# Kernel tuning notes

Hardware: AMD Instinct MI355X
Metric: run time of the kernel (lower is better)

Reference implementation:

```python
import jax, jax.numpy as jnp
import numpy as np

N_NODES = 50000
N_EDGES = 400000
N_GRAPHS = 1024
HEADS = 2
HID = 312


def gat_conv(x, src, dst, W, a_src, a_dst, bias, n):
    # PyG GATConv, concat=False (mean over heads), negative_slope=0.2,
    # self-loops already included in (src, dst). Eval mode (no dropout).
    h = (x @ W).reshape(n, HEADS, -1)                      # [N,H,C]
    s_src = (h * a_src[None]).sum(-1)                      # [N,H]
    s_dst = (h * a_dst[None]).sum(-1)                      # [N,H]
    alpha = jax.nn.leaky_relu(s_src[src] + s_dst[dst], 0.2)  # [E,H]
    m = jax.ops.segment_max(alpha, dst, num_segments=n)
    e = jnp.exp(alpha - m[dst])
    z = jax.ops.segment_sum(e, dst, num_segments=n)
    coef = e / (z[dst] + 1e-16)                            # edge softmax over dst
    msg = h[src] * coef[:, :, None]                        # [E,H,C]
    out = jax.ops.segment_sum(msg, dst, num_segments=n)    # [N,H,C]
    return out.mean(axis=1) + bias


def setup_inputs() -> dict:
    key = jax.random.key(0)
    ks = jax.random.split(key, 32)
    d = {}
    d['mol_x'] = jax.random.normal(ks[0], (N_NODES, 78), jnp.float32)
    d['mol_edge_index'] = jax.random.randint(ks[1], (2, N_EDGES), 0, N_NODES, jnp.int32)
    d['mol_batch'] = jnp.sort(jax.random.randint(ks[2], (N_NODES,), 0, N_GRAPHS, jnp.int32))
    sc = 0.05
    d['W0'] = jax.random.normal(ks[3], (78, HEADS * HID)) * sc
    d['as0'] = jax.random.normal(ks[4], (HEADS, HID)) * sc
    d['ad0'] = jax.random.normal(ks[5], (HEADS, HID)) * sc
    d['b0'] = jax.random.normal(ks[6], (HID,)) * sc
    d['W1'] = jax.random.normal(ks[7], (HID, HEADS * HID)) * sc
    d['as1'] = jax.random.normal(ks[8], (HEADS, HID)) * sc
    d['ad1'] = jax.random.normal(ks[9], (HEADS, HID)) * sc
    d['b1'] = jax.random.normal(ks[10], (HID,)) * sc
    d['W2'] = jax.random.normal(ks[11], (HID, HEADS * HID)) * sc
    d['as2'] = jax.random.normal(ks[12], (HEADS, HID)) * sc
    d['ad2'] = jax.random.normal(ks[13], (HEADS, HID)) * sc
    d['b2'] = jax.random.normal(ks[14], (HID,)) * sc
    d['fc1_w'] = jax.random.normal(ks[15], (HID, HID)) * sc
    d['fc1_b'] = jax.random.normal(ks[16], (HID,)) * sc
    d['fc2_w'] = jax.random.normal(ks[17], (HID, HID)) * sc
    d['fc2_b'] = jax.random.normal(ks[18], (HID,)) * sc
    d['mol_bias'] = jax.random.uniform(ks[19], (1, HID), minval=-0.2, maxval=0.2)
    d['g1_w'] = jax.random.normal(ks[20], (HID, 1024)) * sc
    d['g1_b'] = jax.random.normal(ks[21], (1024,)) * sc
    d['g2_w'] = jax.random.normal(ks[22], (1024, 128)) * sc
    d['g2_b'] = jax.random.normal(ks[23], (128,)) * sc
    return d


def reference(mol_x, mol_edge_index, mol_batch,
              W0, as0, ad0, b0, W1, as1, ad1, b1, W2, as2, ad2, b2,
              fc1_w, fc1_b, fc2_w, fc2_b, mol_bias,
              g1_w, g1_b, g2_w, g2_b):
    n = mol_x.shape[0]
    loops = jnp.arange(n, dtype=mol_edge_index.dtype)
    src = jnp.concatenate([mol_edge_index[0], loops])
    dst = jnp.concatenate([mol_edge_index[1], loops])

    x1 = jax.nn.relu(gat_conv(mol_x, src, dst, W0, as0, ad0, b0, n))
    h = x1
    for (W, a_s, a_d, b, act) in [(W1, as1, ad1, b1, True), (W2, as2, ad2, b2, False)]:
        x = gat_conv(h, src, dst, W, a_s, a_d, b, n)
        if act:
            x = jax.nn.relu(x)
        z = jax.nn.sigmoid(x @ fc1_w + fc1_b + h @ fc2_w + fc2_b + mol_bias)
        h = z * x + (1 - z) * h

    # global mean pool over graphs
    sums = jax.ops.segment_sum(h, mol_batch, num_segments=N_GRAPHS)
    cnt = jax.ops.segment_sum(jnp.ones((n,), h.dtype), mol_batch, num_segments=N_GRAPHS)
    pooled = sums / jnp.maximum(cnt, 1.0)[:, None]

    out = jax.nn.relu(pooled @ g1_w + g1_b)
    out = out @ g2_w + g2_b  # dropout = identity (eval)
    return out
```

## Files before the change

kernel.cpp:

```cpp
#include <hip/hip_runtime.h>
#include <cstdint>
#include <cstddef>

#define NNODES 50000
#define NEDGE0 400000
#define NETOT  450000
#define NGRAPH 1024
#define CH     312
#define HC     624
#define MP     50048
#define KPA    320
#define AST    640
#define KP0    128
#define GW1    1024

typedef __attribute__((ext_vector_type(4))) float f32x4;
typedef __attribute__((ext_vector_type(8))) short s16x8;

__device__ __forceinline__ unsigned short f2bf(float x) {
  union { float f; unsigned u; } v; v.f = x;
  unsigned r = v.u + 0x7fffu + ((v.u >> 16) & 1u);
  return (unsigned short)(r >> 16);
}
__device__ __forceinline__ float bf2f(unsigned short u) {
  union { unsigned u; float f; } v; v.u = ((unsigned)u) << 16;
  return v.f;
}
__device__ __forceinline__ void gl_lds16(const unsigned short* g, unsigned short* l) {
  __builtin_amdgcn_global_load_lds(
      (const __attribute__((address_space(1))) unsigned int*)g,
      (__attribute__((address_space(3))) unsigned int*)l, 16, 0, 0);
}

__global__ void cvt0_k(const float* __restrict__ in, unsigned short* __restrict__ out) {
  int i = blockIdx.x * blockDim.x + threadIdx.x;
  if (i >= MP * KP0) return;
  int n = i >> 7, c = i & 127;
  out[i] = (n < NNODES && c < 78) ? f2bf(in[(size_t)n * 78 + c]) : (unsigned short)0;
}

__global__ void tcast_k(const float* __restrict__ in, unsigned short* __restrict__ out,
                        int K, int N, int KP_, int NP_) {
  int i = blockIdx.x * blockDim.x + threadIdx.x;
  if (i >= NP_ * KP_) return;
  int n = i / KP_, k = i - n * KP_;
  out[i] = (n < N && k < K) ? f2bf(in[(size_t)k * N + n]) : (unsigned short)0;
}

__global__ void combcast_k(const float* __restrict__ W, unsigned short* __restrict__ out,
                           int K, int KX) {
  int i = blockIdx.x * blockDim.x + threadIdx.x;
  int W2 = 2 * KX;
  if (i >= 384 * W2) return;
  int n = i / W2, k = i - n * W2;
  float v = 0.f;
  if (n < CH) {
    int hd = (k >= KX) ? 1 : 0;
    int kk = hd ? k - KX : k;
    if (kk < K) v = 0.5f * W[(size_t)kk * HC + hd * CH + n];
  }
  out[i] = f2bf(v);
}

__global__ void wafill_k(const float* __restrict__ W, const float* __restrict__ a_s,
                         const float* __restrict__ a_d, float* __restrict__ wa,
                         int K, int KX) {
  int tid = blockIdx.x * blockDim.x + threadIdx.x;
  if (tid >= 4 * KX) return;
  int j = tid / KX, k = tid - j * KX;
  int hd = j & 1;
  const float* a = (j < 2) ? a_s : a_d;
  float s = 0.f;
  if (k < K)
    for (int c = 0; c < CH; ++c)
      s += W[(size_t)k * HC + hd * CH + c] * a[hd * CH + c];
  wa[j * KX + k] = s;
}

__global__ void tcast2_k(const float* __restrict__ fc1, const float* __restrict__ fc2,
                         unsigned short* __restrict__ out) {
  int i = blockIdx.x * blockDim.x + threadIdx.x;
  if (i >= 384 * AST) return;
  int n = i / AST, k = i - n * AST;
  float v = 0.f;
  if (n < CH) {
    if (k < CH) v = fc1[(size_t)k * CH + n];
    else if (k >= KPA && k - KPA < CH) v = fc2[(size_t)(k - KPA) * CH + n];
  }
  out[i] = f2bf(v);
}

__global__ void biasprep_k(const float* __restrict__ b0_, const float* __restrict__ b1_,
                           const float* __restrict__ b2_, const float* __restrict__ fc1b,
                           const float* __restrict__ fc2b, const float* __restrict__ mb,
                           float* __restrict__ bp0, float* __restrict__ bp1,
                           float* __restrict__ bp2, float* __restrict__ gb) {
  int i = blockIdx.x * blockDim.x + threadIdx.x;
  if (i >= 4 * KPA) return;
  int seg = i / KPA, c = i - seg * KPA;
  bool in = c < CH;
  if (seg == 0)      bp0[c] = in ? b0_[c] : 0.f;
  else if (seg == 1) bp1[c] = in ? b1_[c] : 0.f;
  else if (seg == 2) bp2[c] = in ? b2_[c] : 0.f;
  else               gb[c]  = in ? (fc1b[c] + fc2b[c] + mb[c]) : 0.f;
}

__global__ __launch_bounds__(256) void gemm_bb(
    const unsigned short* __restrict__ A, int lda,
    const unsigned short* __restrict__ Bt,
    unsigned short* __restrict__ Cb, float* __restrict__ Cf,
    const float* __restrict__ bias,
    const unsigned short* __restrict__ Xg, const unsigned short* __restrict__ Hg,
    int M, int N, int KP_, int ldc, int act, int gx)
{
  const int nwg = gridDim.x, orig = blockIdx.x;
  const int q = nwg >> 3, r = nwg & 7;
  const int xcd = orig & 7, loc = orig >> 3;
  const int swz = (xcd < r ? xcd * (q + 1) : r * (q + 1) + (xcd - r) * q) + loc;
  const int bn = (swz % gx) * 64, bm = (swz / gx) * 128;

  __shared__ __align__(16) char smem[49152];
  unsigned short* As = (unsigned short*)smem;
  unsigned short* Bs = (unsigned short*)(smem + 32768);
  const int tid = threadIdx.x, lane = tid & 63, w = tid >> 6;
  const int rr = lane >> 3;
  const int cc8 = (lane & 7) ^ rr;

  const int nkt = KP_ >> 6;

  auto stage = [&](int b, int kt) {
    #pragma unroll
    for (int i = 0; i < 4; ++i) {
      int R = w * 32 + i * 8;
      gl_lds16(A + (size_t)(bm + R + rr) * lda + kt * 64 + cc8 * 8,
               As + b * 8192 + R * 64);
    }
    #pragma unroll
    for (int i = 0; i < 2; ++i) {
      int R = w * 16 + i * 8;
      gl_lds16(Bt + (size_t)(bn + R + rr) * KP_ + kt * 64 + cc8 * 8,
               Bs + b * 4096 + R * 64);
    }
  };

  const int r16 = lane & 15, g4 = lane >> 4;
  f32x4 zf = {0.f, 0.f, 0.f, 0.f};
  f32x4 acc[2][4];
  #pragma unroll
  for (int m = 0; m < 2; ++m)
    #pragma unroll
    for (int n = 0; n < 4; ++n) acc[m][n] = zf;

  stage(0, 0);
  stage(1, 1);
  int buf = 0;
  for (int kt = 0; kt < nkt; ++kt) {
    if (kt == nkt - 1) asm volatile("s_waitcnt vmcnt(0)" ::: "memory");
    else               asm volatile("s_waitcnt vmcnt(6)" ::: "memory");
    __builtin_amdgcn_s_barrier();
    #pragma unroll
    for (int k2 = 0; k2 < 2; ++k2) {
      s16x8 bfr[4], afr[2];
      #pragma unroll
      for (int n = 0; n < 4; ++n) {
        int rB = n * 16 + r16;
        int ch = (k2 * 4 + g4) ^ (rB & 7);
        bfr[n] = *(const s16x8*)&Bs[buf * 4096 + rB * 64 + ch * 8];
      }
      #pragma unroll
      for (int m = 0; m < 2; ++m) {
        int rA = w * 32 + m * 16 + r16;
        int ch = (k2 * 4 + g4) ^ (rA & 7);
        afr[m] = *(const s16x8*)&As[buf * 8192 + rA * 64 + ch * 8];
      }
      __builtin_amdgcn_s_setprio(1);
      #pragma unroll
      for (int m = 0; m < 2; ++m)
        #pragma unroll
        for (int n = 0; n < 4; ++n)
          acc[m][n] = __builtin_amdgcn_mfma_f32_16x16x32_bf16(afr[m], bfr[n],
                                                              acc[m][n], 0, 0, 0);
      __builtin_amdgcn_s_setprio(0);
    }
    __builtin_amdgcn_s_barrier();
    if (kt + 2 < nkt) stage(buf, kt + 2);
    buf ^= 1;
  }

  float* Ct = (float*)smem;
  #pragma unroll
  for (int m = 0; m < 2; ++m) {
    int row0 = w * 32 + m * 16 + g4 * 4;
    #pragma unroll
    for (int n = 0; n < 4; ++n) {
      int col = n * 16 + r16;
      #pragma unroll
      for (int r2 = 0; r2 < 4; ++r2)
        Ct[(row0 + r2) * 68 + col] = acc[m][n][r2];
    }
  }
  __builtin_amdgcn_s_barrier();

  if (Cf) {
    for (int c = tid; c < 128 * 16; c += 256) {
      int row = c >> 4, c4 = (c & 15) * 4;
      int gm = bm + row, gn = bn + c4;
      if (gm >= M) continue;
      f32x4 v;
      #pragma unroll
      for (int rj = 0; rj < 4; ++rj) {
        float x = Ct[row * 68 + c4 + rj] + bias[gn + rj];
        if (act) x = x > 0.f ? x : 0.f;
        v[rj] = x;
      }
      *(f32x4*)(Cf + (size_t)gm * ldc + gn) = v;
    }
  } else {
    for (int c = tid; c < 128 * 8; c += 256) {
      int row = c >> 3, c8 = (c & 7) * 8;
      int gm = bm + row, gn = bn + c8;
      if (gm >= M) continue;
      size_t obase = (size_t)gm * ldc + gn;
      s16x8 o;
      if (Xg) {
        s16x8 xv = *(const s16x8*)(Xg + obase);
        s16x8 hv = *(const s16x8*)(Hg + obase);
        #pragma unroll
        for (int rj = 0; rj < 8; ++rj) {
          float v = Ct[row * 68 + c8 + rj] + bias[gn + rj];
          float g = 1.f / (1.f + __expf(-v));
          float x = bf2f((unsigned short)xv[rj]);
          float h = bf2f((unsigned short)hv[rj]);
          o[rj] = (short)f2bf(g * x + (1.f - g) * h);
        }
      } else {
        #pragma unroll
        for (int rj = 0; rj < 8; ++rj) {
          float v = Ct[row * 68 + c8 + rj] + bias[gn + rj];
          if (act) v = v > 0.f ? v : 0.f;
          o[rj] = (short)f2bf(v);
        }
      }
      *(s16x8*)(Cb + obase) = o;
    }
  }
}

__global__ void hist_k(const int* __restrict__ ei, int* __restrict__ cnt) {
  int e = blockIdx.x * blockDim.x + threadIdx.x;
  if (e >= NETOT) return;
  int d = (e < NEDGE0) ? ei[NEDGE0 + e] : e - NEDGE0;
  atomicAdd(&cnt[d], 1);
}

__global__ __launch_bounds__(1024) void scan_k(const int* __restrict__ cnt,
                                               int* __restrict__ rowptr) {
  __shared__ int wsum[16];
  __shared__ int carry_s;
  int t = threadIdx.x, lane = t & 63, wv = t >> 6;
  if (t == 0) carry_s = 0;
  __syncthreads();
  for (int base = 0; base < NNODES; base += 1024) {
    int idx = base + t;
    int v = (idx < NNODES) ? cnt[idx] : 0;
    int s = v;
    #pragma unroll
    for (int off = 1; off < 64; off <<= 1) {
      int x = __shfl_up(s, off);
      if (lane >= off) s += x;
    }
    if (lane == 63) wsum[wv] = s;
    __syncthreads();
    if (wv == 0) {
      int ws = (lane < 16) ? wsum[lane] : 0;
      #pragma unroll
      for (int off = 1; off < 16; off <<= 1) {
        int x = __shfl_up(ws, off);
        if (lane >= off) ws += x;
      }
      if (lane < 16) wsum[lane] = ws;
    }
    __syncthreads();
    int carry = carry_s;
    int woff = wv ? wsum[wv - 1] : 0;
    if (idx < NNODES) rowptr[idx] = carry + woff + s - v;
    __syncthreads();
    if (t == 1023) carry_s = carry + wsum[15];
    __syncthreads();
  }
  if (t == 0) rowptr[NNODES] = carry_s;
}

__global__ void scatter_k(const int* __restrict__ ei, const int* __restrict__ rowptr,
                          int* __restrict__ cur, int* __restrict__ esrc) {
  int e = blockIdx.x * blockDim.x + threadIdx.x;
  if (e >= NETOT) return;
  int s, d;
  if (e < NEDGE0) { s = ei[e]; d = ei[NEDGE0 + e]; }
  else { s = d = e - NEDGE0; }
  int pos = rowptr[d] + atomicAdd(&cur[d], 1);
  esrc[pos] = s;
}

template<int NCH>
__global__ __launch_bounds__(256) void scoresX_k(
    const unsigned short* __restrict__ X, int stride,
    const float* __restrict__ wa, float* __restrict__ Sc)
{
  int wid = (blockIdx.x * blockDim.x + threadIdx.x) >> 6;
  int lane = threadIdx.x & 63;
  if (wid >= NNODES) return;
  const int K = NCH * 8;
  float d[4] = {0, 0, 0, 0};
  if (lane < NCH) {
    s16x8 xv = *(const s16x8*)(X + (size_t)wid * stride + lane * 8);
    float xf[8];
    #pragma unroll
    for (int r = 0; r < 8; ++r) xf[r] = bf2f((unsigned short)xv[r]);
    #pragma unroll
    for (int j = 0; j < 4; ++j) {
      const float* wp = wa + j * K + lane * 8;
      float s = 0.f;
      #pragma unroll
      for (int r = 0; r < 8; ++r) s += xf[r] * wp[r];
      d[j] = s;
    }
  }
  #pragma unroll
  for (int off = 32; off; off >>= 1) {
    #pragma unroll
    for (int j = 0; j < 4; ++j) d[j] += __shfl_xor(d[j], off);
  }
  if (lane == 0) {
    f32x4 v = {d[0], d[1], d[2], d[3]};
    *(f32x4*)(Sc + (size_t)wid * 4) = v;
  }
}

template<int NCH>
__global__ __launch_bounds__(256) void msgX_k(
    const int* __restrict__ rowptr, const int* __restrict__ esrc,
    const float* __restrict__ Sc, const unsigned short* __restrict__ X,
    int stride, unsigned short* __restrict__ xagg)
{
  int wid = (blockIdx.x * blockDim.x + threadIdx.x) >> 6;
  int lane = threadIdx.x & 63;
  if (wid >= NNODES) return;
  int e0 = rowptr[wid], e1 = rowptr[wid + 1];
  float sd0 = Sc[(size_t)wid * 4 + 2], sd1 = Sc[(size_t)wid * 4 + 3];

  float m0 = -1e30f, m1 = -1e30f, z0 = 0.f, z1 = 0.f;
  for (int base = e0; base < e1; base += 64) {
    int cnt = e1 - base; if (cnt > 64) cnt = 64;
    float a0 = -1e30f, a1 = -1e30f;
    if (lane < cnt) {
      int sl = esrc[base + lane];
      f32x4 sv = *(const f32x4*)(Sc + (size_t)sl * 4);
      a0 = sv[0] + sd0; a0 = a0 > 0.f ? a0 : 0.2f * a0;
      a1 = sv[1] + sd1; a1 = a1 > 0.f ? a1 : 0.2f * a1;
    }
    float cm0 = a0, cm1 = a1;
    #pragma unroll
    for (int off = 32; off; off >>= 1) {
      cm0 = fmaxf(cm0, __shfl_xor(cm0, off));
      cm1 = fmaxf(cm1, __shfl_xor(cm1, off));
    }
    float nm0 = fmaxf(m0, cm0), nm1 = fmaxf(m1, cm1);
    z0 *= __expf(m0 - nm0); z1 *= __expf(m1 - nm1);
    m0 = nm0; m1 = nm1;
    float w0 = (lane < cnt) ? __expf(a0 - m0) : 0.f;
    float w1 = (lane < cnt) ? __expf(a1 - m1) : 0.f;
    #pragma unroll
    for (int off = 32; off; off >>= 1) {
      w0 += __shfl_xor(w0, off);
      w1 += __shfl_xor(w1, off);
    }
    z0 += w0; z1 += w1;
  }
  float i0 = 1.f / (z0 + 1e-16f), i1 = 1.f / (z1 + 1e-16f);

  float a0h[8] = {0,0,0,0,0,0,0,0};
  float a1h[8] = {0,0,0,0,0,0,0,0};

  for (int base = e0; base < e1; base += 64) {
    int cnt = e1 - base; if (cnt > 64) cnt = 64;
    int sl = 0;
    float c0 = 0.f, c1 = 0.f;
    if (lane < cnt) {
      sl = esrc[base + lane];
      f32x4 sv = *(const f32x4*)(Sc + (size_t)sl * 4);
      float a0 = sv[0] + sd0; a0 = a0 > 0.f ? a0 : 0.2f * a0;
      float a1 = sv[1] + sd1; a1 = a1 > 0.f ? a1 : 0.2f * a1;
      c0 = __expf(a0 - m0) * i0;
      c1 = __expf(a1 - m1) * i1;
    }
    if (NCH == 40) {
      for (int e = 0; e < cnt; ++e) {
        int   s  = __shfl(sl, e);
        float w0 = __shfl(c0, e), w1 = __shfl(c1, e);
        if (lane < NCH) {
          s16x8 xv = *(const s16x8*)(X + (size_t)s * stride + lane * 8);
          #pragma unroll
          for (int r = 0; r < 8; ++r) {
            float xf = bf2f((unsigned short)xv[r]);
            a0h[r] += w0 * xf;
            a1h[r] += w1 * xf;
          }
        }
      }
    } else {
      for (int e = 0; e < cnt; e += 4) {
        int ee = e + (lane >> 4);
        bool on = ee < cnt;
        int   s  = __shfl(sl, on ? ee : e);
        float w0 = __shfl(c0, on ? ee : e), w1 = __shfl(c1, on ? ee : e);
        if (on) {
          s16x8 xv = *(const s16x8*)(X + (size_t)s * stride + (lane & 15) * 8);
          #pragma unroll
          for (int r = 0; r < 8; ++r) {
            float xf = bf2f((unsigned short)xv[r]);
            a0h[r] += w0 * xf;
            a1h[r] += w1 * xf;
          }
        }
      }
    }
  }

  if (NCH == 16) {
    #pragma unroll
    for (int r = 0; r < 8; ++r) {
      a0h[r] += __shfl_xor(a0h[r], 16); a0h[r] += __shfl_xor(a0h[r], 32);
      a1h[r] += __shfl_xor(a1h[r], 16); a1h[r] += __shfl_xor(a1h[r], 32);
    }
  }
  if (lane < NCH) {
    s16x8 o0, o1;
    #pragma unroll
    for (int r = 0; r < 8; ++r) {
      o0[r] = (short)f2bf(a0h[r]);
      o1[r] = (short)f2bf(a1h[r]);
    }
    unsigned short* op = xagg + (size_t)wid * (2 * NCH * 8);
    *(s16x8*)(op + lane * 8) = o0;
    *(s16x8*)(op + NCH * 8 + lane * 8) = o1;
  }
}

__global__ void gptr_k(const int* __restrict__ batch, int* __restrict__ gptr) {
  int g = blockIdx.x * blockDim.x + threadIdx.x;
  if (g > NGRAPH) return;
  int lo = 0, hi = NNODES;
  while (lo < hi) { int mid = (lo + hi) >> 1; if (batch[mid] < g) lo = mid + 1; else hi = mid; }
  gptr[g] = lo;
}

__global__ __launch_bounds__(256) void pool_k(const unsigned short* __restrict__ hs,
                                              const int* __restrict__ gptr,
                                              unsigned short* __restrict__ pooled) {
  int g = blockIdx.x;
  int n0 = gptr[g], n1 = gptr[g + 1];
  float inv = (n1 > n0) ? 1.f / (float)(n1 - n0) : 0.f;
  for (int c = threadIdx.x; c < KPA; c += 256) {
    float s = 0.f;
    if (c < CH)
      for (int n = n0; n < n1; ++n) s += bf2f(hs[(size_t)n * AST + c]);
    pooled[(size_t)g * KPA + c] = f2bf(s * inv);
  }
}

extern "C" void kernel_launch(void* const* d_in, const int* in_sizes, int n_in,
                              void* d_out, int out_size, void* d_ws, size_t ws_size,
                              hipStream_t stream)
{
  const float* mol_x = (const float*)d_in[0];
  const int*   ei    = (const int*)d_in[1];
  const int*   batch = (const int*)d_in[2];
  const float* W0  = (const float*)d_in[3];
  const float* as0 = (const float*)d_in[4];
  const float* ad0 = (const float*)d_in[5];
  const float* b0  = (const float*)d_in[6];
  const float* W1  = (const float*)d_in[7];
  const float* as1 = (const float*)d_in[8];
  const float* ad1 = (const float*)d_in[9];
  const float* b1  = (const float*)d_in[10];
  const float* W2  = (const float*)d_in[11];
  const float* as2 = (const float*)d_in[12];
  const float* ad2 = (const float*)d_in[13];
  const float* b2  = (const float*)d_in[14];
  const float* fc1w = (const float*)d_in[15];
  const float* fc1b = (const float*)d_in[16];
  const float* fc2w = (const float*)d_in[17];
  const float* fc2b = (const float*)d_in[18];
  const float* mbias = (const float*)d_in[19];
  const float* g1w = (const float*)d_in[20];
  const float* g1b = (const float*)d_in[21];
  const float* g2w = (const float*)d_in[22];
  const float* g2b = (const float*)d_in[23];
  float* out = (float*)d_out;

  char* ws = (char*)d_ws;
  size_t off = 0;
  auto alloc = [&](size_t b) { size_t r = off; off += (b + 255) & ~(size_t)255; return r; };
  unsigned short* xagg = (unsigned short*)(ws + alloc((size_t)MP * AST * 2));
  unsigned short* actA = (unsigned short*)(ws + alloc((size_t)MP * AST * 2));
  unsigned short* actB = (unsigned short*)(ws + alloc((size_t)MP * AST * 2));
  unsigned short* xb0  = (unsigned short*)(ws + alloc((size_t)MP * KP0 * 2));
  float* Sc     = (float*)(ws + alloc((size_t)MP * 4 * 4));
  int*   cnt    = (int*)(ws + alloc((size_t)2 * NNODES * 4));
  int*   cnt2   = cnt + NNODES;
  int*   rowptr = (int*)(ws + alloc((size_t)(NNODES + 1) * 4));
  int*   esrc   = (int*)(ws + alloc((size_t)NETOT * 4));
  int*   gptr   = (int*)(ws + alloc((size_t)(NGRAPH + 1) * 4));
  float* gbias  = (float*)(ws + alloc((size_t)KPA * 4));
  float* bp0    = (float*)(ws + alloc((size_t)KPA * 4));
  float* bp1    = (float*)(ws + alloc((size_t)KPA * 4));
  float* bp2    = (float*)(ws + alloc((size_t)KPA * 4));
  float* wa0    = (float*)(ws + alloc((size_t)4 * KP0 * 4));
  float* wa1    = (float*)(ws + alloc((size_t)4 * KPA * 4));
  float* wa2    = (float*)(ws + alloc((size_t)4 * KPA * 4));
  unsigned short* pooled_b = (unsigned short*)(ws + alloc((size_t)NGRAPH * KPA * 2));
  unsigned short* gbuf_b   = (unsigned short*)(ws + alloc((size_t)NGRAPH * GW1 * 2));
  unsigned short* comb0t = (unsigned short*)(ws + alloc((size_t)384 * 256 * 2));
  unsigned short* comb1t = (unsigned short*)(ws + alloc((size_t)384 * AST * 2));
  unsigned short* comb2t = (unsigned short*)(ws + alloc((size_t)384 * AST * 2));
  unsigned short* fc12t  = (unsigned short*)(ws + alloc((size_t)384 * AST * 2));
  unsigned short* g1t    = (unsigned short*)(ws + alloc((size_t)GW1 * KPA * 2));
  unsigned short* g2t    = (unsigned short*)(ws + alloc((size_t)128 * GW1 * 2));

  hipMemsetAsync(cnt, 0, (size_t)2 * NNODES * 4, stream);
  hist_k<<<(NETOT + 255) / 256, 256, 0, stream>>>(ei, cnt);
  scan_k<<<1, 1024, 0, stream>>>(cnt, rowptr);
  scatter_k<<<(NETOT + 255) / 256, 256, 0, stream>>>(ei, rowptr, cnt2, esrc);
  gptr_k<<<(NGRAPH + 256) / 256, 256, 0, stream>>>(batch, gptr);
  cvt0_k<<<(MP * KP0 + 255) / 256, 256, 0, stream>>>(mol_x, xb0);
  combcast_k<<<(384 * 256 + 255) / 256, 256, 0, stream>>>(W0, comb0t, 78, KP0);
  combcast_k<<<(384 * AST + 255) / 256, 256, 0, stream>>>(W1, comb1t, CH, KPA);
  combcast_k<<<(384 * AST + 255) / 256, 256, 0, stream>>>(W2, comb2t, CH, KPA);
  wafill_k<<<(4 * KP0 + 255) / 256, 256, 0, stream>>>(W0, as0, ad0, wa0, 78, KP0);
  wafill_k<<<(4 * KPA + 255) / 256, 256, 0, stream>>>(W1, as1, ad1, wa1, CH, KPA);
  wafill_k<<<(4 * KPA + 255) / 256, 256, 0, stream>>>(W2, as2, ad2, wa2, CH, KPA);
  tcast2_k<<<(384 * AST + 255) / 256, 256, 0, stream>>>(fc1w, fc2w, fc12t);
  biasprep_k<<<(4 * KPA + 255) / 256, 256, 0, stream>>>(b0, b1, b2, fc1b, fc2b, mbias,
                                                        bp0, bp1, bp2, gbias);
  tcast_k<<<(GW1 * KPA + 255) / 256, 256, 0, stream>>>(g1w, g1t, CH, GW1, KPA, GW1);
  tcast_k<<<(128 * GW1 + 255) / 256, 256, 0, stream>>>(g2w, g2t, GW1, 128, GW1, 128);

  auto mgemm = [&](const unsigned short* A, int lda, const unsigned short* Bt,
                   unsigned short* Cb, float* Cf, const float* bias,
                   const unsigned short* Xg, const unsigned short* Hg,
                   int M, int N, int KP_, int ldc, int act) {
    int gx = (N + 63) / 64, gy = (M + 127) / 128;
    hipLaunchKernelGGL(gemm_bb, dim3(gx * gy), dim3(256), 0, stream, A, lda, Bt,
                       Cb, Cf, bias, Xg, Hg, M, N, KP_, ldc, act, gx);
  };

  const int MSGB = (NNODES * 64 + 255) / 256;
  unsigned short* hA = actA + KPA;
  unsigned short* hB = actB + KPA;

  scoresX_k<16><<<MSGB, 256, 0, stream>>>(xb0, KP0, wa0, Sc);
  msgX_k<16><<<MSGB, 256, 0, stream>>>(rowptr, esrc, Sc, xb0, KP0, xagg);
  mgemm(xagg, 256, comb0t, hA, nullptr, bp0, nullptr, nullptr,
        NNODES, KPA, 256, AST, 1);

  scoresX_k<40><<<MSGB, 256, 0, stream>>>(hA, AST, wa1, Sc);
  msgX_k<40><<<MSGB, 256, 0, stream>>>(rowptr, esrc, Sc, hA, AST, xagg);
  mgemm(xagg, AST, comb1t, actA, nullptr, bp1, nullptr, nullptr,
        NNODES, KPA, AST, AST, 1);
  mgemm(actA, AST, fc12t, hB, nullptr, gbias, actA, hA,
        NNODES, KPA, AST, AST, 0);

  scoresX_k<40><<<MSGB, 256, 0, stream>>>(hB, AST, wa2, Sc);
  msgX_k<40><<<MSGB, 256, 0, stream>>>(rowptr, esrc, Sc, hB, AST, xagg);
  mgemm(xagg, AST, comb2t, actB, nullptr, bp2, nullptr, nullptr,
        NNODES, KPA, AST, AST, 0);
  mgemm(actB, AST, fc12t, hA, nullptr, gbias, actB, hB,
        NNODES, KPA, AST, AST, 0);

  pool_k<<<NGRAPH, 256, 0, stream>>>(hA, gptr, pooled_b);
  mgemm(pooled_b, KPA, g1t, gbuf_b, nullptr, g1b, nullptr, nullptr,
        NGRAPH, GW1, KPA, GW1, 1);
  mgemm(gbuf_b, GW1, g2t, nullptr, out, g2b, nullptr, nullptr,
        NGRAPH, 128, GW1, 128, 0);
}
```

Measured before the change: 601.7 us.

## Split edge softmax and aggregation into separate kernels with per-thread channel slices

The fused message kernel, which used one wavefront per node with serialized per-edge shuffles and idle lanes, is split in two. The first kernel computes the softmax coefficients per edge and stores them as packed fp16 pairs. The second kernel gives each thread one 8-channel chunk of one node and loops over its edges, spreading the channel dimension across 8 block slices for better lane utilization and occupancy. This costs an extra launch per layer and an extra pass over the edge list and coefficients, and the fp16 coefficients lose some precision.

```diff
diff --git a/kernel.cpp b/kernel.cpp
--- a/kernel.cpp
+++ b/kernel.cpp
@@ -16,6 +16,7 @@
 
 typedef __attribute__((ext_vector_type(4))) float f32x4;
 typedef __attribute__((ext_vector_type(8))) short s16x8;
+typedef decltype(__builtin_amdgcn_cvt_pkrtz(0.f, 0.f)) pk16x2;
 
 __device__ __forceinline__ unsigned short f2bf(float x) {
   union { float f; unsigned u; } v; v.f = x;
@@ -337,11 +338,9 @@
   }
 }
 
-template<int NCH>
-__global__ __launch_bounds__(256) void msgX_k(
+__global__ __launch_bounds__(256) void mzcoef_k(
     const int* __restrict__ rowptr, const int* __restrict__ esrc,
-    const float* __restrict__ Sc, const unsigned short* __restrict__ X,
-    int stride, unsigned short* __restrict__ xagg)
+    const float* __restrict__ Sc, unsigned* __restrict__ ecoef)
 {
   int wid = (blockIdx.x * blockDim.x + threadIdx.x) >> 6;
   int lane = threadIdx.x & 63;
@@ -379,72 +378,61 @@
   }
   float i0 = 1.f / (z0 + 1e-16f), i1 = 1.f / (z1 + 1e-16f);
 
-  float a0h[8] = {0,0,0,0,0,0,0,0};
-  float a1h[8] = {0,0,0,0,0,0,0,0};
-
   for (int base = e0; base < e1; base += 64) {
     int cnt = e1 - base; if (cnt > 64) cnt = 64;
-    int sl = 0;
-    float c0 = 0.f, c1 = 0.f;
     if (lane < cnt) {
-      sl = esrc[base + lane];
+      int sl = esrc[base + lane];
       f32x4 sv = *(const f32x4*)(Sc + (size_t)sl * 4);
       float a0 = sv[0] + sd0; a0 = a0 > 0.f ? a0 : 0.2f * a0;
       float a1 = sv[1] + sd1; a1 = a1 > 0.f ? a1 : 0.2f * a1;
-      c0 = __expf(a0 - m0) * i0;
-      c1 = __expf(a1 - m1) * i1;
-    }
-    if (NCH == 40) {
-      for (int e = 0; e < cnt; ++e) {
-        int   s  = __shfl(sl, e);
-        float w0 = __shfl(c0, e), w1 = __shfl(c1, e);
-        if (lane < NCH) {
-          s16x8 xv = *(const s16x8*)(X + (size_t)s * stride + lane * 8);
-          #pragma unroll
-          for (int r = 0; r < 8; ++r) {
-            float xf = bf2f((unsigned short)xv[r]);
-            a0h[r] += w0 * xf;
-            a1h[r] += w1 * xf;
-          }
-        }
-      }
-    } else {
-      for (int e = 0; e < cnt; e += 4) {
-        int ee = e + (lane >> 4);
-        bool on = ee < cnt;
-        int   s  = __shfl(sl, on ? ee : e);
-        float w0 = __shfl(c0, on ? ee : e), w1 = __shfl(c1, on ? ee : e);
-        if (on) {
-          s16x8 xv = *(const s16x8*)(X + (size_t)s * stride + (lane & 15) * 8);
-          #pragma unroll
-          for (int r = 0; r < 8; ++r) {
-            float xf = bf2f((unsigned short)xv[r]);
-            a0h[r] += w0 * xf;
-            a1h[r] += w1 * xf;
-          }
-        }
-      }
-    }
-  }
-
-  if (NCH == 16) {
+      float c0 = __expf(a0 - m0) * i0;
+      float c1 = __expf(a1 - m1) * i1;
+      union { pk16x2 h2; unsigned u; } u;
+      u.h2 = __builtin_amdgcn_cvt_pkrtz(c0, c1);
+      ecoef[base + lane] = u.u;
+    }
+  }
+}
+
+template<int NCH>
+__global__ __launch_bounds__(256) void aggX_k(
+    const int* __restrict__ rowptr, const int* __restrict__ esrc,
+    const unsigned* __restrict__ ecoef, const unsigned short* __restrict__ X,
+    int stride, unsigned short* __restrict__ xagg)
+{
+  const int CPS = NCH / 8;
+  const int NPB = 256 / CPS;
+  int slice = blockIdx.x & 7;
+  int nb    = blockIdx.x >> 3;
+  int t = threadIdx.x;
+  int local = t / CPS, cp = t - local * CPS;
+  int n = nb * NPB + local;
+  if (local >= NPB || n >= NNODES) return;
+  int chunk = slice * CPS + cp;
+  int e0 = rowptr[n], e1 = rowptr[n + 1];
+  const unsigned short* xp = X + chunk * 8;
+  float a0[8] = {0,0,0,0,0,0,0,0}, a1[8] = {0,0,0,0,0,0,0,0};
+  for (int e = e0; e < e1; ++e) {
+    int s = esrc[e];
+    union { unsigned u; _Float16 h[2]; } uc; uc.u = ecoef[e];
+    float w0 = (float)uc.h[0], w1 = (float)uc.h[1];
+    s16x8 xv = *(const s16x8*)(xp + (size_t)s * stride);
     #pragma unroll
     for (int r = 0; r < 8; ++r) {
-      a0h[r] += __shfl_xor(a0h[r], 16); a0h[r] += __shfl_xor(a0h[r], 32);
-      a1h[r] += __shfl_xor(a1h[r], 16); a1h[r] += __shfl_xor(a1h[r], 32);
-    }
-  }
-  if (lane < NCH) {
-    s16x8 o0, o1;
-    #pragma unroll
-    for (int r = 0; r < 8; ++r) {
-      o0[r] = (short)f2bf(a0h[r]);
-      o1[r] = (short)f2bf(a1h[r]);
-    }
-    unsigned short* op = xagg + (size_t)wid * (2 * NCH * 8);
-    *(s16x8*)(op + lane * 8) = o0;
-    *(s16x8*)(op + NCH * 8 + lane * 8) = o1;
-  }
+      float xf = bf2f((unsigned short)xv[r]);
+      a0[r] += w0 * xf;
+      a1[r] += w1 * xf;
+    }
+  }
+  s16x8 o0, o1;
+  #pragma unroll
+  for (int r = 0; r < 8; ++r) {
+    o0[r] = (short)f2bf(a0[r]);
+    o1[r] = (short)f2bf(a1[r]);
+  }
+  unsigned short* op = xagg + (size_t)n * (2 * NCH * 8) + chunk * 8;
+  *(s16x8*)op = o0;
+  *(s16x8*)(op + NCH * 8) = o1;
 }
 
 __global__ void gptr_k(const int* __restrict__ batch, int* __restrict__ gptr) {
@@ -507,6 +495,7 @@
   unsigned short* actB = (unsigned short*)(ws + alloc((size_t)MP * AST * 2));
   unsigned short* xb0  = (unsigned short*)(ws + alloc((size_t)MP * KP0 * 2));
   float* Sc     = (float*)(ws + alloc((size_t)MP * 4 * 4));
+  unsigned* ecoef = (unsigned*)(ws + alloc((size_t)NETOT * 4));
   int*   cnt    = (int*)(ws + alloc((size_t)2 * NNODES * 4));
   int*   cnt2   = cnt + NNODES;
   int*   rowptr = (int*)(ws + alloc((size_t)(NNODES + 1) * 4));
@@ -556,23 +545,28 @@
   };
 
   const int MSGB = (NNODES * 64 + 255) / 256;
+  const int AGG16 = ((NNODES + 127) / 128) * 8;
+  const int AGG40 = ((NNODES + 50) / 51) * 8;
   unsigned short* hA = actA + KPA;
   unsigned short* hB = actB + KPA;
 
   scoresX_k<16><<<MSGB, 256, 0, stream>>>(xb0, KP0, wa0, Sc);
-  msgX_k<16><<<MSGB, 256, 0, stream>>>(rowptr, esrc, Sc, xb0, KP0, xagg);
+  mzcoef_k<<<MSGB, 256, 0, stream>>>(rowptr, esrc, Sc, ecoef);
+  aggX_k<16><<<AGG16, 256, 0, stream>>>(rowptr, esrc, ecoef, xb0, KP0, xagg);
   mgemm(xagg, 256, comb0t, hA, nullptr, bp0, nullptr, nullptr,
         NNODES, KPA, 256, AST, 1);
 
   scoresX_k<40><<<MSGB, 256, 0, stream>>>(hA, AST, wa1, Sc);
-  msgX_k<40><<<MSGB, 256, 0, stream>>>(rowptr, esrc, Sc, hA, AST, xagg);
+  mzcoef_k<<<MSGB, 256, 0, stream>>>(rowptr, esrc, Sc, ecoef);
+  aggX_k<40><<<AGG40, 256, 0, stream>>>(rowptr, esrc, ecoef, hA, AST, xagg);
   mgemm(xagg, AST, comb1t, actA, nullptr, bp1, nullptr, nullptr,
         NNODES, KPA, AST, AST, 1);
   mgemm(actA, AST, fc12t, hB, nullptr, gbias, actA, hA,
         NNODES, KPA, AST, AST, 0);
 
   scoresX_k<40><<<MSGB, 256, 0, stream>>>(hB, AST, wa2, Sc);
-  msgX_k<40><<<MSGB, 256, 0, stream>>>(rowptr, esrc, Sc, hB, AST, xagg);
+  mzcoef_k<<<MSGB, 256, 0, stream>>>(rowptr, esrc, Sc, ecoef);
+  aggX_k<40><<<AGG40, 256, 0, stream>>>(rowptr, esrc, ecoef, hB, AST, xagg);
   mgemm(xagg, AST, comb2t, actB, nullptr, bp2, nullptr, nullptr,
         NNODES, KPA, AST, AST, 0);
   mgemm(actB, AST, fc12t, hA, nullptr, gbias, actB, hB,
```

After: 789.0 us. 1.31x slower.
